# Kernel optimization log

Hardware: AMD Instinct MI355X
Metric: run time of the kernel (lower is better)

## Reference

```python
import jax, jax.numpy as jnp
import numpy as np

N = 50000   # nodes
E = 800000  # edges (avg degree 16)
IN = 128
H = 128
OUT = 16
BN_EPS = 1e-5


def _uniform(key, shape, fan_in):
    s = 1.0 / np.sqrt(fan_in)
    return jax.random.uniform(key, shape, jnp.float32, -s, s)


def setup_inputs() -> dict:
    key = jax.random.key(0)
    ks = jax.random.split(key, 12)
    x = jax.random.normal(ks[0], (N, IN), jnp.float32)
    edge_index = jax.random.randint(ks[1], (2, E), 0, N, dtype=jnp.int64)
    # SAGEConv layer 1: lin_l (with bias) on aggregated neighbors, lin_r (no bias) on root
    Wl1 = _uniform(ks[2], (H, IN), IN)
    bl1 = _uniform(ks[3], (H,), IN)
    Wr1 = _uniform(ks[4], (H, IN), IN)
    # SAGEConv layer 2
    Wl2 = _uniform(ks[5], (OUT, H), H)
    bl2 = _uniform(ks[6], (OUT,), H)
    Wr2 = _uniform(ks[7], (OUT, H), H)
    # BatchNorm1d(H) affine params
    gamma = jnp.ones((H,), jnp.float32)
    beta = jnp.zeros((H,), jnp.float32)
    # PReLU single shared slope
    a = jnp.array(0.25, jnp.float32)
    return {"x": x, "edge_index": edge_index, "Wl1": Wl1, "bl1": bl1, "Wr1": Wr1,
            "Wl2": Wl2, "bl2": bl2, "Wr2": Wr2, "gamma": gamma, "beta": beta, "a": a}


def sage_conv(x, src, dst, Wl, bl, Wr):
    # mean-aggregate source features at destination nodes
    msg = x[src]                                              # [E, F] gather
    summ = jax.ops.segment_sum(msg, dst, num_segments=N)      # [N, F] scatter-add
    cnt = jax.ops.segment_sum(jnp.ones((src.shape[0],), x.dtype), dst, num_segments=N)
    agg = summ / jnp.clip(cnt, 1.0)[:, None]
    return agg @ Wl.T + bl + x @ Wr.T


def reference(x, edge_index, Wl1, bl1, Wr1, Wl2, bl2, Wr2, gamma, beta, a):
    src, dst = edge_index[0], edge_index[1]
    # layer 1: SAGEConv -> BatchNorm (batch stats) -> PReLU -> residual
    h = sage_conv(x, src, dst, Wl1, bl1, Wr1)
    mean = h.mean(axis=0)
    var = h.var(axis=0)  # biased, as in torch BN training
    h = gamma * (h - mean) / jnp.sqrt(var + BN_EPS) + beta
    h = jnp.where(h >= 0, h, a * h)  # PReLU (shared slope)
    h = h + x  # residual (hidden == in)
    # layer 2 + log_softmax over classes
    out = sage_conv(h, src, dst, Wl2, bl2, Wr2)
    return jax.nn.log_softmax(out, axis=1)
```

## Files before the change

### kernel.cpp

```cpp
#include <hip/hip_runtime.h>

#define NNODES 50000
#define EEDGES 800000
#define FIN 128
#define FH 128
#define FOUT 16
#define BN_EPS 1e-5f
#define NBIN 391
#define CAP 4096
#define PCH 2048
#define NPB 391
#define NTILES 1563
#define PACKBLKS 3143

typedef short bf16x8 __attribute__((ext_vector_type(8)));
typedef float f32x4 __attribute__((ext_vector_type(4)));

__device__ inline unsigned short tobf16(float f) {
    unsigned int u = __float_as_uint(f);
    u += 0x7fffu + ((u >> 16) & 1u);
    return (unsigned short)(u >> 16);
}
__device__ inline float frombf16(unsigned short h) {
    return __uint_as_float(((unsigned int)h) << 16);
}
__device__ inline unsigned packbf(float f0, float f1) {
    return (unsigned)tobf16(f0) | ((unsigned)tobf16(f1) << 16);
}
__device__ inline float lo16(unsigned u) { return __uint_as_float(u << 16); }
__device__ inline float hi16(unsigned u) { return __uint_as_float(u & 0xffff0000u); }

__global__ void part_pack_kernel(const int* __restrict__ src, const int* __restrict__ dst,
                                 int* __restrict__ binFill, unsigned int* __restrict__ edgeBin,
                                 const float* __restrict__ x,
                                 const float* __restrict__ Wl1, const float* __restrict__ Wr1,
                                 const float* __restrict__ Wl2, const float* __restrict__ Wr2,
                                 unsigned short* __restrict__ xb, unsigned short* __restrict__ wb) {
    __shared__ int hist[NBIN];
    __shared__ int runBase[NBIN];
    __shared__ int runFill[NBIN];
    int t = threadIdx.x;
    if (blockIdx.x < NPB) {
        for (int i = t; i < NBIN; i += 256) { hist[i] = 0; runFill[i] = 0; }
        __syncthreads();
        int e0 = blockIdx.x * PCH;
        for (int i = 0; i < PCH / 256; ++i) {
            int e = e0 + i * 256 + t;
            if (e < EEDGES) atomicAdd(&hist[dst[e] >> 7], 1);
        }
        __syncthreads();
        for (int i = t; i < NBIN; i += 256) {
            int c = hist[i];
            if (c) runBase[i] = atomicAdd(&binFill[i], c);
        }
        __syncthreads();
        for (int i = 0; i < PCH / 256; ++i) {
            int e = e0 + i * 256 + t;
            if (e < EEDGES) {
                int d = dst[e];
                int b = d >> 7;
                int off = runBase[b] + atomicAdd(&runFill[b], 1);
                if (off < CAP)
                    edgeBin[(size_t)b * CAP + off] = ((unsigned)(d & 127) << 17) | (unsigned)src[e];
            }
        }
    } else {
        int tt = (blockIdx.x - NPB) * 256 + t;
        int base = tt * 8;
        const float* srcp;
        unsigned short* dstp;
        int off;
        if (base < NNODES * FIN) {
            srcp = x; off = base; dstp = xb + base;
        } else {
            int w = base - NNODES * FIN;
            if (w >= 36864) return;
            dstp = wb + w;
            if (w < 16384)      { srcp = Wl1; off = w; }
            else if (w < 32768) { srcp = Wr1; off = w - 16384; }
            else if (w < 34816) { srcp = Wl2; off = w - 32768; }
            else                { srcp = Wr2; off = w - 34816; }
        }
        float4 f0 = *reinterpret_cast<const float4*>(srcp + off);
        float4 f1 = *reinterpret_cast<const float4*>(srcp + off + 4);
        uint4 r;
        r.x = packbf(f0.x, f0.y);
        r.y = packbf(f0.z, f0.w);
        r.z = packbf(f1.x, f1.y);
        r.w = packbf(f1.z, f1.w);
        *reinterpret_cast<uint4*>(dstp) = r;
    }
}

__global__ void binscan_scan_kernel(const unsigned int* __restrict__ edgeBin,
                                    const int* __restrict__ binFill,
                                    int* __restrict__ localPrefix,
                                    int* __restrict__ binOff) {
    int t = threadIdx.x;
    if (blockIdx.x < NBIN) {
        __shared__ int cnt[128];
        __shared__ int sc[128];
        int b = blockIdx.x;
        if (t < 128) cnt[t] = 0;
        __syncthreads();
        int n = binFill[b];
        for (int k = t; k < n; k += 256)
            atomicAdd(&cnt[edgeBin[(size_t)b * CAP + k] >> 17], 1);
        __syncthreads();
        if (t < 128) sc[t] = cnt[t];
        __syncthreads();
        for (int off = 1; off < 128; off <<= 1) {
            int v = (t < 128 && t >= off) ? sc[t - off] : 0;
            __syncthreads();
            if (t < 128) sc[t] += v;
            __syncthreads();
        }
        if (t < 128) localPrefix[b * 128 + t] = sc[t] - cnt[t];
    } else {
        __shared__ int sh[512];
        int v0 = (t < NBIN) ? binFill[t] : 0;
        int v1 = (t + 256 < NBIN) ? binFill[t + 256] : 0;
        sh[t] = v0; sh[t + 256] = v1;
        __syncthreads();
        for (int off = 1; off < 512; off <<= 1) {
            int a0 = (t >= off) ? sh[t - off] : 0;
            int a1 = (t + 256 >= off) ? sh[t + 256 - off] : 0;
            __syncthreads();
            sh[t] += a0; sh[t + 256] += a1;
            __syncthreads();
        }
        if (t < NBIN) binOff[t] = sh[t] - v0;
        if (t + 256 < NBIN) binOff[t + 256] = sh[t + 256] - v1;
    }
}

__global__ void local_bucket_kernel(const unsigned int* __restrict__ edgeBin,
                                    const int* __restrict__ binFill,
                                    const int* __restrict__ binOff,
                                    const int* __restrict__ localPrefix,
                                    int* __restrict__ srcSorted,
                                    int* __restrict__ rowstart) {
    __shared__ int wp[128];
    int b = blockIdx.x;
    int t = threadIdx.x;
    if (t < 128) {
        int node = b * 128 + t;
        int rs = binOff[b] + localPrefix[b * 128 + t];
        wp[t] = rs;
        if (node < NNODES) rowstart[node] = rs;
    }
    if (b == 0 && t == 128) rowstart[NNODES] = EEDGES;
    __syncthreads();
    int n = binFill[b];
    for (int k = t; k < n; k += 256) {
        unsigned c = edgeBin[(size_t)b * CAP + k];
        int p = atomicAdd(&wp[c >> 17], 1);
        srcSorted[p] = (int)(c & 0x1FFFF);
    }
}

__global__ void gather_bf16(const unsigned short* __restrict__ feat,
                            const int* __restrict__ rowstart,
                            const int* __restrict__ srcSorted,
                            unsigned short* __restrict__ aggout) {
    int tid = threadIdx.x;
    int i = blockIdx.x * 4 + (tid >> 6);
    int j = tid & 63;
    const unsigned int* fp = (const unsigned int*)feat;
    int k0 = rowstart[i], k1 = rowstart[i + 1];
    float a0 = 0.0f, a1 = 0.0f;
    int k = k0;
    for (; k + 8 <= k1; k += 8) {
        int s0 = srcSorted[k],     s1 = srcSorted[k + 1], s2 = srcSorted[k + 2], s3 = srcSorted[k + 3];
        int s4 = srcSorted[k + 4], s5 = srcSorted[k + 5], s6 = srcSorted[k + 6], s7 = srcSorted[k + 7];
        unsigned int u0 = fp[(size_t)s0 * 64 + j];
        unsigned int u1 = fp[(size_t)s1 * 64 + j];
        unsigned int u2 = fp[(size_t)s2 * 64 + j];
        unsigned int u3 = fp[(size_t)s3 * 64 + j];
        unsigned int u4 = fp[(size_t)s4 * 64 + j];
        unsigned int u5 = fp[(size_t)s5 * 64 + j];
        unsigned int u6 = fp[(size_t)s6 * 64 + j];
        unsigned int u7 = fp[(size_t)s7 * 64 + j];
        a0 += lo16(u0) + lo16(u1) + lo16(u2) + lo16(u3) + lo16(u4) + lo16(u5) + lo16(u6) + lo16(u7);
        a1 += hi16(u0) + hi16(u1) + hi16(u2) + hi16(u3) + hi16(u4) + hi16(u5) + hi16(u6) + hi16(u7);
    }
    for (; k + 4 <= k1; k += 4) {
        int s0 = srcSorted[k], s1 = srcSorted[k + 1], s2 = srcSorted[k + 2], s3 = srcSorted[k + 3];
        unsigned int u0 = fp[(size_t)s0 * 64 + j];
        unsigned int u1 = fp[(size_t)s1 * 64 + j];
        unsigned int u2 = fp[(size_t)s2 * 64 + j];
        unsigned int u3 = fp[(size_t)s3 * 64 + j];
        a0 += lo16(u0) + lo16(u1) + lo16(u2) + lo16(u3);
        a1 += hi16(u0) + hi16(u1) + hi16(u2) + hi16(u3);
    }
    for (; k < k1; ++k) {
        unsigned int u = fp[(size_t)srcSorted[k] * 64 + j];
        a0 += lo16(u);
        a1 += hi16(u);
    }
    float inv = 1.0f / (float)max(k1 - k0, 1);
    ((unsigned int*)aggout)[(size_t)i * 64 + j] = packbf(a0 * inv, a1 * inv);
}

__global__ void __launch_bounds__(256, 2)
lin1_persist(const unsigned short* __restrict__ aggb,
             const unsigned short* __restrict__ xb,
             const unsigned short* __restrict__ wl,
             const unsigned short* __restrict__ wr,
             const float* __restrict__ bias,
             unsigned short* __restrict__ hb,
             float* __restrict__ bnsum, float* __restrict__ bnsq) {
    __shared__ float bps[128];
    __shared__ float bpq[128];
    int tid = threadIdx.x;
    if (tid < 128) { bps[tid] = 0.0f; bpq[tid] = 0.0f; }
    __syncthreads();
    int wave = tid >> 6;
    int lane = tid & 63;
    int c = wave & 1;
    int rsub = wave >> 1;
    int lrow = lane & 15;
    int kg = lane >> 4;

    bf16x8 wlF[4][4], wrF[4][4];
    #pragma unroll
    for (int nf = 0; nf < 4; ++nf) {
        #pragma unroll
        for (int ks = 0; ks < 4; ++ks) {
            wlF[nf][ks] = *(const bf16x8*)(wl + (size_t)(c * 64 + nf * 16 + lrow) * 128 + ks * 32 + kg * 8);
            wrF[nf][ks] = *(const bf16x8*)(wr + (size_t)(c * 64 + nf * 16 + lrow) * 128 + ks * 32 + kg * 8);
        }
    }
    float bias_v[4];
    #pragma unroll
    for (int nf = 0; nf < 4; ++nf) bias_v[nf] = bias[c * 64 + nf * 16 + lrow];

    for (int tIt = blockIdx.x; tIt < NTILES; tIt += gridDim.x) {
        int rowA = tIt * 32 + rsub * 16 + lrow;
        int arow = min(rowA, NNODES - 1);
        bf16x8 aA[4], aX[4];
        #pragma unroll
        for (int ks = 0; ks < 4; ++ks) {
            aA[ks] = *(const bf16x8*)(aggb + (size_t)arow * 128 + ks * 32 + kg * 8);
            aX[ks] = *(const bf16x8*)(xb + (size_t)arow * 128 + ks * 32 + kg * 8);
        }
        f32x4 acc[4] = {};
        #pragma unroll
        for (int ks = 0; ks < 4; ++ks) {
            #pragma unroll
            for (int nf = 0; nf < 4; ++nf) {
                acc[nf] = __builtin_amdgcn_mfma_f32_16x16x32_bf16(aA[ks], wlF[nf][ks], acc[nf], 0, 0, 0);
                acc[nf] = __builtin_amdgcn_mfma_f32_16x16x32_bf16(aX[ks], wrF[nf][ks], acc[nf], 0, 0, 0);
            }
        }
        #pragma unroll
        for (int nf = 0; nf < 4; ++nf) {
            float s = 0.0f, q = 0.0f;
            #pragma unroll
            for (int rr = 0; rr < 4; ++rr) {
                int row = tIt * 32 + rsub * 16 + kg * 4 + rr;
                if (row < NNODES) {
                    unsigned short hv = tobf16(acc[nf][rr] + bias_v[nf]);
                    float vr = frombf16(hv);
                    hb[(size_t)row * 128 + c * 64 + nf * 16 + lrow] = hv;
                    s += vr; q += vr * vr;
                }
            }
            s += __shfl_xor(s, 16); s += __shfl_xor(s, 32);
            q += __shfl_xor(q, 16); q += __shfl_xor(q, 32);
            if (lane < 16) {
                atomicAdd(&bps[c * 64 + nf * 16 + lane], s);
                atomicAdd(&bpq[c * 64 + nf * 16 + lane], q);
            }
        }
    }
    __syncthreads();
    if (tid < 128) {
        atomicAdd(&bnsum[tid], bps[tid]);
        atomicAdd(&bnsq[tid], bpq[tid]);
    }
}

__global__ void bn_lin2a_kernel(unsigned short* __restrict__ hb,
                                const unsigned short* __restrict__ xb,
                                const float* __restrict__ gamma, const float* __restrict__ beta,
                                const float* __restrict__ aptr,
                                const float* __restrict__ bnsum, const float* __restrict__ bnsq,
                                const unsigned short* __restrict__ wl,
                                unsigned short* __restrict__ y2) {
    __shared__ float scs[128];
    __shared__ float shs[128];
    int tid = threadIdx.x;
    if (tid < 128) {
        const float invN = 1.0f / (float)NNODES;
        float mean = bnsum[tid] * invN;
        float var = bnsq[tid] * invN - mean * mean;
        float istd = rsqrtf(var + BN_EPS);
        float sc = gamma[tid] * istd;
        scs[tid] = sc;
        shs[tid] = beta[tid] - mean * sc;
    }
    __syncthreads();
    float aP = aptr[0];
    int wave = tid >> 6;
    int lane = tid & 63;
    int row0 = blockIdx.x * 64 + wave * 16;
    int lrow = lane & 15;
    int kg = lane >> 4;
    int rowA = row0 + lrow;
    int arow = min(rowA, NNODES - 1);
    f32x4 acc = {};
    #pragma unroll
    for (int ks = 0; ks < 4; ++ks) {
        bf16x8 hv = *(const bf16x8*)(hb + (size_t)arow * 128 + ks * 32 + kg * 8);
        bf16x8 xv = *(const bf16x8*)(xb + (size_t)arow * 128 + ks * 32 + kg * 8);
        bf16x8 nv;
        #pragma unroll
        for (int e = 0; e < 8; ++e) {
            int f = ks * 32 + kg * 8 + e;
            float v = frombf16((unsigned short)hv[e]) * scs[f] + shs[f];
            v = (v >= 0.0f) ? v : aP * v;
            v += frombf16((unsigned short)xv[e]);
            nv[e] = (short)tobf16(v);
        }
        if (rowA < NNODES)
            *(bf16x8*)(hb + (size_t)arow * 128 + ks * 32 + kg * 8) = nv;
        bf16x8 b = *(const bf16x8*)(wl + (size_t)lrow * 128 + ks * 32 + kg * 8);
        acc = __builtin_amdgcn_mfma_f32_16x16x32_bf16(nv, b, acc, 0, 0, 0);
    }
    #pragma unroll
    for (int r = 0; r < 4; ++r) {
        int row = row0 + kg * 4 + r;
        if (row < NNODES)
            y2[(size_t)row * 16 + lrow] = tobf16(acc[r]);
    }
}

__global__ void gather16_kernel(const unsigned short* __restrict__ y2,
                                const int* __restrict__ rowstart,
                                const int* __restrict__ srcSorted,
                                unsigned short* __restrict__ agg2) {
    int tid = threadIdx.x;
    int i = blockIdx.x * 4 + (tid >> 6);
    int lane = tid & 63;
    int e = lane >> 3;
    int j = lane & 7;
    const unsigned int* yp = (const unsigned int*)y2;
    int k0 = rowstart[i], k1 = rowstart[i + 1];
    float a0 = 0.0f, a1 = 0.0f;
    for (int k = k0; k < k1; k += 8) {
        int kk = k + e;
        if (kk < k1) {
            unsigned u = yp[(size_t)srcSorted[kk] * 8 + j];
            a0 += lo16(u);
            a1 += hi16(u);
        }
    }
    a0 += __shfl_xor(a0, 8);  a1 += __shfl_xor(a1, 8);
    a0 += __shfl_xor(a0, 16); a1 += __shfl_xor(a1, 16);
    a0 += __shfl_xor(a0, 32); a1 += __shfl_xor(a1, 32);
    if (e == 0) {
        float inv = 1.0f / (float)max(k1 - k0, 1);
        ((unsigned int*)agg2)[(size_t)i * 8 + j] = packbf(a0 * inv, a1 * inv);
    }
}

__global__ void lin2b_kernel(const unsigned short* __restrict__ agg2,
                             const unsigned short* __restrict__ hb,
                             const unsigned short* __restrict__ wr,
                             const float* __restrict__ bias,
                             float* __restrict__ out) {
    int wave = threadIdx.x >> 6;
    int lane = threadIdx.x & 63;
    int row0 = blockIdx.x * 64 + wave * 16;
    int lrow = lane & 15;
    int kg = lane >> 4;
    int arow = min(row0 + lrow, NNODES - 1);
    f32x4 acc = {};
    #pragma unroll
    for (int ks = 0; ks < 4; ++ks) {
        bf16x8 a = *(const bf16x8*)(hb + (size_t)arow * 128 + ks * 32 + kg * 8);
        bf16x8 b = *(const bf16x8*)(wr + (size_t)lrow * 128 + ks * 32 + kg * 8);
        acc = __builtin_amdgcn_mfma_f32_16x16x32_bf16(a, b, acc, 0, 0, 0);
    }
    float bl = bias[lrow];
    #pragma unroll
    for (int r = 0; r < 4; ++r) {
        int row = row0 + kg * 4 + r;
        int rowc = min(row, NNODES - 1);
        float v = acc[r] + bl + frombf16(agg2[(size_t)rowc * 16 + lrow]);
        float m = v;
        for (int s = 1; s < 16; s <<= 1) m = fmaxf(m, __shfl_xor(m, s, 16));
        float ex = expf(v - m);
        float se = ex;
        for (int s = 1; s < 16; s <<= 1) se += __shfl_xor(se, s, 16);
        if (row < NNODES)
            out[(size_t)row * FOUT + lrow] = v - m - logf(se);
    }
}

extern "C" void kernel_launch(void* const* d_in, const int* in_sizes, int n_in,
                              void* d_out, int out_size, void* d_ws, size_t ws_size,
                              hipStream_t stream) {
    const float* x    = (const float*)d_in[0];
    const int*   ei   = (const int*)d_in[1];
    const int*   src  = ei;
    const int*   dst  = ei + EEDGES;
    const float* Wl1  = (const float*)d_in[2];
    const float* bl1  = (const float*)d_in[3];
    const float* Wr1  = (const float*)d_in[4];
    const float* Wl2  = (const float*)d_in[5];
    const float* bl2  = (const float*)d_in[6];
    const float* Wr2  = (const float*)d_in[7];
    const float* gamma= (const float*)d_in[8];
    const float* beta = (const float*)d_in[9];
    const float* a    = (const float*)d_in[10];
    float* out = (float*)d_out;

    char* W = (char*)d_ws;
    unsigned short* xb    = (unsigned short*)(W + 0);
    unsigned short* hb    = (unsigned short*)(W + 12800000);
    unsigned int*  edgeBin= (unsigned int*)(W + 25600000);
    unsigned short* aggb  = (unsigned short*)(W + 25600000);
    unsigned short* y2b   = (unsigned short*)(W + 25600000);
    unsigned short* agg2b = (unsigned short*)(W + 27200000);
    unsigned short* wb    = (unsigned short*)(W + 38400000);
    int* binFill  = (int*)(W + 38473728);
    float* bnsum  = (float*)(W + 38475292);
    float* bnsq   = (float*)(W + 38475804);
    int* binOff   = (int*)(W + 38476316);
    int* localPrefix = (int*)(W + 38477880);
    int* rowstart = (int*)(W + 38678072);
    int* srcSorted= (int*)(W + 38878076);

    unsigned short* wl1b = wb;
    unsigned short* wr1b = wb + 16384;
    unsigned short* wl2b = wb + 32768;
    unsigned short* wr2b = wb + 34816;

    hipMemsetAsync(binFill, 0, (size_t)2588, stream);

    part_pack_kernel<<<NPB + PACKBLKS, 256, 0, stream>>>(src, dst, binFill, edgeBin,
                                                         x, Wl1, Wr1, Wl2, Wr2, xb, wb);
    binscan_scan_kernel<<<NBIN + 1, 256, 0, stream>>>(edgeBin, binFill, localPrefix, binOff);
    local_bucket_kernel<<<NBIN, 256, 0, stream>>>(edgeBin, binFill, binOff, localPrefix,
                                                  srcSorted, rowstart);

    gather_bf16<<<NNODES / 4, 256, 0, stream>>>(xb, rowstart, srcSorted, aggb);
    lin1_persist<<<512, 256, 0, stream>>>(aggb, xb, wl1b, wr1b, bl1, hb, bnsum, bnsq);

    bn_lin2a_kernel<<<782, 256, 0, stream>>>(hb, xb, gamma, beta, a, bnsum, bnsq, wl2b, y2b);

    gather16_kernel<<<NNODES / 4, 256, 0, stream>>>(y2b, rowstart, srcSorted, agg2b);
    lin2b_kernel<<<782, 256, 0, stream>>>(agg2b, hb, wr2b, bl2, out);
}
```

Measured before the change: 141.9 us.

## Fuse bucket scan passes and merge second gather with output linear

Merges the bin-scan and local-bucket kernels into one kernel. Each block computes its bin offset by reducing the preceding bins' fills and caches its edges in shared memory, so edgeBin is read once instead of twice. Fuses the layer-2 neighbor gather with the final linear and log-softmax kernel, keeping aggregated values in shared memory in fp32 instead of writing and reading a bf16 buffer. It also enlarges the partition chunk size, cutting the partition block count. In exchange, the fused gather uses fewer blocks that each process 64 nodes serially per wave, which lowers parallelism for latency-bound gathers.

```diff
diff --git a/kernel.cpp b/kernel.cpp
--- a/kernel.cpp
+++ b/kernel.cpp
@@ -8,8 +8,8 @@
 #define BN_EPS 1e-5f
 #define NBIN 391
 #define CAP 4096
-#define PCH 2048
-#define NPB 391
+#define PCH 8192
+#define NPB 98
 #define NTILES 1563
 #define PACKBLKS 3143
 
@@ -92,68 +92,55 @@
     }
 }
 
-__global__ void binscan_scan_kernel(const unsigned int* __restrict__ edgeBin,
+__global__ void bucket_fused_kernel(const unsigned int* __restrict__ edgeBin,
                                     const int* __restrict__ binFill,
-                                    int* __restrict__ localPrefix,
-                                    int* __restrict__ binOff) {
-    int t = threadIdx.x;
-    if (blockIdx.x < NBIN) {
-        __shared__ int cnt[128];
-        __shared__ int sc[128];
-        int b = blockIdx.x;
-        if (t < 128) cnt[t] = 0;
-        __syncthreads();
-        int n = binFill[b];
-        for (int k = t; k < n; k += 256)
-            atomicAdd(&cnt[edgeBin[(size_t)b * CAP + k] >> 17], 1);
-        __syncthreads();
-        if (t < 128) sc[t] = cnt[t];
-        __syncthreads();
-        for (int off = 1; off < 128; off <<= 1) {
-            int v = (t < 128 && t >= off) ? sc[t - off] : 0;
-            __syncthreads();
-            if (t < 128) sc[t] += v;
-            __syncthreads();
-        }
-        if (t < 128) localPrefix[b * 128 + t] = sc[t] - cnt[t];
-    } else {
-        __shared__ int sh[512];
-        int v0 = (t < NBIN) ? binFill[t] : 0;
-        int v1 = (t + 256 < NBIN) ? binFill[t + 256] : 0;
-        sh[t] = v0; sh[t + 256] = v1;
-        __syncthreads();
-        for (int off = 1; off < 512; off <<= 1) {
-            int a0 = (t >= off) ? sh[t - off] : 0;
-            int a1 = (t + 256 >= off) ? sh[t + 256 - off] : 0;
-            __syncthreads();
-            sh[t] += a0; sh[t + 256] += a1;
-            __syncthreads();
-        }
-        if (t < NBIN) binOff[t] = sh[t] - v0;
-        if (t + 256 < NBIN) binOff[t + 256] = sh[t + 256] - v1;
-    }
-}
-
-__global__ void local_bucket_kernel(const unsigned int* __restrict__ edgeBin,
-                                    const int* __restrict__ binFill,
-                                    const int* __restrict__ binOff,
-                                    const int* __restrict__ localPrefix,
                                     int* __restrict__ srcSorted,
                                     int* __restrict__ rowstart) {
+    __shared__ unsigned eb[CAP];
+    __shared__ int cnt[128];
+    __shared__ int sc[128];
     __shared__ int wp[128];
+    __shared__ int wsum[4];
     int b = blockIdx.x;
     int t = threadIdx.x;
+
+    int contrib = 0;
+    if (t < NBIN && t < b) contrib += binFill[t];
+    int t2 = t + 256;
+    if (t2 < NBIN && t2 < b) contrib += binFill[t2];
+    for (int off = 32; off; off >>= 1) contrib += __shfl_down(contrib, off, 64);
+    if ((t & 63) == 0) wsum[t >> 6] = contrib;
+    if (t < 128) cnt[t] = 0;
+    __syncthreads();
+    int binOffB = wsum[0] + wsum[1] + wsum[2] + wsum[3];
+
+    int n = min(binFill[b], CAP);
+    for (int k = t; k < n; k += 256) {
+        unsigned c = edgeBin[(size_t)b * CAP + k];
+        eb[k] = c;
+        atomicAdd(&cnt[c >> 17], 1);
+    }
+    __syncthreads();
+
+    if (t < 128) sc[t] = cnt[t];
+    __syncthreads();
+    for (int off = 1; off < 128; off <<= 1) {
+        int v = (t < 128 && t >= off) ? sc[t - off] : 0;
+        __syncthreads();
+        if (t < 128) sc[t] += v;
+        __syncthreads();
+    }
     if (t < 128) {
         int node = b * 128 + t;
-        int rs = binOff[b] + localPrefix[b * 128 + t];
+        int rs = binOffB + sc[t] - cnt[t];
         wp[t] = rs;
         if (node < NNODES) rowstart[node] = rs;
     }
     if (b == 0 && t == 128) rowstart[NNODES] = EEDGES;
     __syncthreads();
-    int n = binFill[b];
+
     for (int k = t; k < n; k += 256) {
-        unsigned c = edgeBin[(size_t)b * CAP + k];
+        unsigned c = eb[k];
         int p = atomicAdd(&wp[c >> 17], 1);
         srcSorted[p] = (int)(c & 0x1FFFF);
     }
@@ -336,45 +323,49 @@
     }
 }
 
-__global__ void gather16_kernel(const unsigned short* __restrict__ y2,
-                                const int* __restrict__ rowstart,
-                                const int* __restrict__ srcSorted,
-                                unsigned short* __restrict__ agg2) {
-    int tid = threadIdx.x;
-    int i = blockIdx.x * 4 + (tid >> 6);
-    int lane = tid & 63;
+__global__ void gather16_lin2b_kernel(const unsigned short* __restrict__ y2,
+                                      const int* __restrict__ rowstart,
+                                      const int* __restrict__ srcSorted,
+                                      const unsigned short* __restrict__ hb,
+                                      const unsigned short* __restrict__ wr,
+                                      const float* __restrict__ bias,
+                                      float* __restrict__ out) {
+    __shared__ float agg[64][16];
+    int t = threadIdx.x;
+    int w = t >> 6;
+    int lane = t & 63;
     int e = lane >> 3;
     int j = lane & 7;
     const unsigned int* yp = (const unsigned int*)y2;
-    int k0 = rowstart[i], k1 = rowstart[i + 1];
-    float a0 = 0.0f, a1 = 0.0f;
-    for (int k = k0; k < k1; k += 8) {
-        int kk = k + e;
-        if (kk < k1) {
-            unsigned u = yp[(size_t)srcSorted[kk] * 8 + j];
-            a0 += lo16(u);
-            a1 += hi16(u);
-        }
-    }
-    a0 += __shfl_xor(a0, 8);  a1 += __shfl_xor(a1, 8);
-    a0 += __shfl_xor(a0, 16); a1 += __shfl_xor(a1, 16);
-    a0 += __shfl_xor(a0, 32); a1 += __shfl_xor(a1, 32);
-    if (e == 0) {
-        float inv = 1.0f / (float)max(k1 - k0, 1);
-        ((unsigned int*)agg2)[(size_t)i * 8 + j] = packbf(a0 * inv, a1 * inv);
-    }
-}
-
-__global__ void lin2b_kernel(const unsigned short* __restrict__ agg2,
-                             const unsigned short* __restrict__ hb,
-                             const unsigned short* __restrict__ wr,
-                             const float* __restrict__ bias,
-                             float* __restrict__ out) {
-    int wave = threadIdx.x >> 6;
-    int lane = threadIdx.x & 63;
-    int row0 = blockIdx.x * 64 + wave * 16;
+    int nodeBase = blockIdx.x * 64;
+
+    for (int it = 0; it < 16; ++it) {
+        int i = nodeBase + w * 16 + it;
+        int ic = min(i, NNODES - 1);
+        int k0 = rowstart[ic], k1 = rowstart[ic + 1];
+        float a0 = 0.0f, a1 = 0.0f;
+        for (int k = k0; k < k1; k += 8) {
+            int kk = k + e;
+            if (kk < k1) {
+                unsigned u = yp[(size_t)srcSorted[kk] * 8 + j];
+                a0 += lo16(u);
+                a1 += hi16(u);
+            }
+        }
+        a0 += __shfl_xor(a0, 8);  a1 += __shfl_xor(a1, 8);
+        a0 += __shfl_xor(a0, 16); a1 += __shfl_xor(a1, 16);
+        a0 += __shfl_xor(a0, 32); a1 += __shfl_xor(a1, 32);
+        if (e == 0) {
+            float inv = 1.0f / (float)max(k1 - k0, 1);
+            agg[w * 16 + it][2 * j]     = a0 * inv;
+            agg[w * 16 + it][2 * j + 1] = a1 * inv;
+        }
+    }
+    __syncthreads();
+
     int lrow = lane & 15;
     int kg = lane >> 4;
+    int row0 = nodeBase + w * 16;
     int arow = min(row0 + lrow, NNODES - 1);
     f32x4 acc = {};
     #pragma unroll
@@ -387,8 +378,8 @@
     #pragma unroll
     for (int r = 0; r < 4; ++r) {
         int row = row0 + kg * 4 + r;
-        int rowc = min(row, NNODES - 1);
-        float v = acc[r] + bl + frombf16(agg2[(size_t)rowc * 16 + lrow]);
+        int lr = w * 16 + kg * 4 + r;
+        float v = acc[r] + bl + agg[lr][lrow];
         float m = v;
         for (int s = 1; s < 16; s <<= 1) m = fmaxf(m, __shfl_xor(m, s, 16));
         float ex = expf(v - m);
@@ -423,13 +414,10 @@
     unsigned int*  edgeBin= (unsigned int*)(W + 25600000);
     unsigned short* aggb  = (unsigned short*)(W + 25600000);
     unsigned short* y2b   = (unsigned short*)(W + 25600000);
-    unsigned short* agg2b = (unsigned short*)(W + 27200000);
     unsigned short* wb    = (unsigned short*)(W + 38400000);
     int* binFill  = (int*)(W + 38473728);
     float* bnsum  = (float*)(W + 38475292);
     float* bnsq   = (float*)(W + 38475804);
-    int* binOff   = (int*)(W + 38476316);
-    int* localPrefix = (int*)(W + 38477880);
     int* rowstart = (int*)(W + 38678072);
     int* srcSorted= (int*)(W + 38878076);
 
@@ -442,15 +430,12 @@
 
     part_pack_kernel<<<NPB + PACKBLKS, 256, 0, stream>>>(src, dst, binFill, edgeBin,
                                                          x, Wl1, Wr1, Wl2, Wr2, xb, wb);
-    binscan_scan_kernel<<<NBIN + 1, 256, 0, stream>>>(edgeBin, binFill, localPrefix, binOff);
-    local_bucket_kernel<<<NBIN, 256, 0, stream>>>(edgeBin, binFill, binOff, localPrefix,
-                                                  srcSorted, rowstart);
+    bucket_fused_kernel<<<NBIN, 256, 0, stream>>>(edgeBin, binFill, srcSorted, rowstart);
 
     gather_bf16<<<NNODES / 4, 256, 0, stream>>>(xb, rowstart, srcSorted, aggb);
     lin1_persist<<<512, 256, 0, stream>>>(aggb, xb, wl1b, wr1b, bl1, hb, bnsum, bnsq);
 
     bn_lin2a_kernel<<<782, 256, 0, stream>>>(hb, xb, gamma, beta, a, bnsum, bnsq, wl2b, y2b);
 
-    gather16_kernel<<<NNODES / 4, 256, 0, stream>>>(y2b, rowstart, srcSorted, agg2b);
-    lin2b_kernel<<<782, 256, 0, stream>>>(agg2b, hb, wr2b, bl2, out);
-}
+    gather16_lin2b_kernel<<<782, 256, 0, stream>>>(y2b, rowstart, srcSorted, hb, wr2b, bl2, out);
+}
```

New measurement: 156.7 us. +10.4%, slower.
